# Kernel optimization log

Hardware: AMD Instinct MI355X
Metric: run time of the kernel (lower is better)

The kernel has to match this reference:

```python
import jax, jax.numpy as jnp
import numpy as np

# dims (see shape_source)
B, NC, DIM_IN = 4, 4095, 64      # batch, cells, invariant state dim (n-6)
D, H, L, K = 128, 4, 2, 6        # d_model, heads, layers, num_neighbors
DH = D // H                      # dim_head = 32
HR, NRBF = 16, 16                # radial hidden dim (d_model//8), rbf basis
RBF_MAX, RBF_W = 4.0, 0.25


def _ln(x, s, b):
    m = x.mean(-1, keepdims=True)
    v = x.var(-1, keepdims=True)
    return (x - m) / jnp.sqrt(v + 1e-5) * s + b


def setup_inputs() -> dict:
    key = jax.random.key(0)
    ks = jax.random.split(key, 32)
    def nrm(k, shape, scale):
        return jax.random.normal(k, shape, jnp.float32) * scale
    p = {}
    p['X'] = nrm(ks[0], (B, NC, 6 + DIM_IN), 1.0)
    p['W_embed'] = nrm(ks[1], (DIM_IN, D), DIM_IN ** -0.5)
    p['b_embed'] = jnp.zeros((D,), jnp.float32)
    p['Wq'] = nrm(ks[2], (L, D, D), D ** -0.5)
    p['Wk'] = nrm(ks[3], (L, D, D), D ** -0.5)
    p['Wv'] = nrm(ks[4], (L, D, D), D ** -0.5)
    p['Wvv'] = nrm(ks[5], (L, D, D), D ** -0.5)
    p['rw1'] = nrm(ks[6], (L, NRBF, HR), NRBF ** -0.5)
    p['rb1'] = jnp.zeros((L, HR), jnp.float32)
    p['rw2'] = nrm(ks[7], (L, HR, 2 * D), HR ** -0.5)
    p['rb2'] = jnp.zeros((L, 2 * D), jnp.float32)
    p['Wo'] = nrm(ks[8], (L, D, D), D ** -0.5)
    p['Wov'] = nrm(ks[9], (L, D, D), D ** -0.5)
    p['ff_w1'] = nrm(ks[10], (L, D, 2 * D), D ** -0.5)
    p['ff_b1'] = jnp.zeros((L, 2 * D), jnp.float32)
    p['ff_w2'] = nrm(ks[11], (L, 2 * D, D), (2 * D) ** -0.5)
    p['ff_b2'] = jnp.zeros((L, D), jnp.float32)
    p['gate_w'] = nrm(ks[12], (L, D, D), D ** -0.5)
    p['gate_b'] = jnp.zeros((L, D), jnp.float32)
    p['ln1_s'] = jnp.ones((L, D), jnp.float32)
    p['ln1_b'] = jnp.zeros((L, D), jnp.float32)
    p['ln2_s'] = jnp.ones((L, D), jnp.float32)
    p['ln2_b'] = jnp.zeros((L, D), jnp.float32)
    p['W_state'] = nrm(ks[13], (D, DIM_IN), D ** -0.5)
    p['b_state'] = jnp.zeros((DIM_IN,), jnp.float32)
    p['W_force'] = nrm(ks[14], (D, 1), D ** -0.5)
    p['b_force'] = jnp.zeros((1,), jnp.float32)
    return p


def _forward(X, W_embed, b_embed, Wq, Wk, Wv, Wvv, rw1, rb1, rw2, rb2, Wo, Wov,
             ff_w1, ff_b1, ff_w2, ff_b2, gate_w, gate_b,
             ln1_s, ln1_b, ln2_s, ln2_b, W_state, b_state, W_force, b_force):
    N = NC + 1  # one extra zero node prepended, as in the torch wrapper
    pos = jnp.concatenate([jnp.zeros((B, 1, 3), X.dtype), X[:, :, 0:3]], axis=1)       # [B,N,3]
    feats = jnp.concatenate([jnp.zeros((B, 1, DIM_IN), X.dtype), X[:, :, 6:]], axis=1)  # [B,N,dim_in]

    # k-nearest-neighbor graph (indices are non-differentiable constants)
    d2 = jnp.sum((pos[:, :, None, :] - pos[:, None, :, :]) ** 2, axis=-1)  # [B,N,N]
    d2 = d2 + jnp.eye(N, dtype=X.dtype) * 1e9                               # exclude self
    _, idx = jax.lax.top_k(-d2, K)                                           # [B,N,K]

    gat = lambda a: jax.vmap(lambda ai, ii: ai[ii])(a, idx)  # [B,N,...] -> [B,N,K,...]

    rel = gat(pos) - pos[:, :, None, :]                      # [B,N,K,3]
    dist = jnp.sqrt(jnp.sum(rel ** 2, axis=-1) + 1e-8)       # [B,N,K]
    u = rel / dist[..., None]                                # unit vectors (degree-1 SH)
    centers = jnp.linspace(0.0, RBF_MAX, NRBF).astype(X.dtype)
    rbf = jnp.exp(-((dist[..., None] - centers) / RBF_W) ** 2)  # [B,N,K,NRBF]

    x0 = feats @ W_embed + b_embed                           # type-0 (invariant) feats
    x1 = jnp.zeros((B, N, D, 3), X.dtype)                    # type-1 (vector) feats

    for l in range(L):
        h = _ln(x0, ln1_s[l], ln1_b[l])
        q = (h @ Wq[l]).reshape(B, N, H, DH)
        kj = gat(h @ Wk[l]).reshape(B, N, K, H, DH)
        vj = gat(h @ Wv[l])                                   # [B,N,K,D]
        # radial MLP on distances -> invariant edge weights
        rad = jax.nn.silu(rbf @ rw1[l] + rb1[l]) @ rw2[l] + rb2[l]  # [B,N,K,2D]
        rg, rv = rad[..., :D], rad[..., D:]
        bias = rg.reshape(B, N, K, H, DH).mean(-1)            # [B,N,K,H]
        logits = jnp.einsum('bnhd,bnkhd->bnhk', q, kj) / np.float32(np.sqrt(DH))
        logits = logits + bias.transpose(0, 1, 3, 2)
        attn = jax.nn.softmax(logits, axis=-1)                # over K neighbors
        # degree-0 messages
        m0 = (vj * jax.nn.silu(rv)).reshape(B, N, K, H, DH)
        out0 = jnp.einsum('bnhk,bnkhd->bnhd', attn, m0).reshape(B, N, D)
        x0 = x0 + out0 @ Wo[l]
        # degree-1 messages: channel-mixed neighbor vectors + radial-weighted unit dirs
        x1j = gat(x1)                                          # [B,N,K,D,3]
        m1 = jnp.einsum('bnkdc,de->bnkec', x1j, Wvv[l]) + rv[..., None] * u[:, :, :, None, :]
        m1 = m1.reshape(B, N, K, H, DH, 3)
        out1 = jnp.einsum('bnhk,bnkhdc->bnhdc', attn, m1).reshape(B, N, D, 3)
        x1 = x1 + jnp.einsum('bndc,de->bnec', out1, Wov[l])
        # feed-forward on invariants + invariant gating of vectors (equivariant)
        h2 = _ln(x0, ln2_s[l], ln2_b[l])
        x0 = x0 + jax.nn.silu(h2 @ ff_w1[l] + ff_b1[l]) @ ff_w2[l] + ff_b2[l]
        x1 = x1 * jax.nn.sigmoid(h2 @ gate_w[l] + gate_b[l])[..., None]

    y0 = x0[:, 1:]                                            # drop extra node
    y1 = jnp.swapaxes(x1[:, 1:], -1, -2)                      # [B,NC,3,D]
    state_update = y0 @ W_state + b_state                     # [B,NC,dim_in]
    forces = (y1 @ W_force + b_force)[..., 0]                 # [B,NC,3]
    forces = forces - forces.mean(axis=1, keepdims=True)      # remove net force
    return state_update, forces


def reference(X, W_embed, b_embed, Wq, Wk, Wv, Wvv, rw1, rb1, rw2, rb2, Wo, Wov,
              ff_w1, ff_b1, ff_w2, ff_b2, gate_w, gate_b,
              ln1_s, ln1_b, ln2_s, ln2_b, W_state, b_state, W_force, b_force):
    return _forward(X, W_embed, b_embed, Wq, Wk, Wv, Wvv, rw1, rb1, rw2, rb2, Wo, Wov,
                    ff_w1, ff_b1, ff_w2, ff_b2, gate_w, gate_b,
                    ln1_s, ln1_b, ln2_s, ln2_b, W_state, b_state, W_force, b_force)
```

## Files before the change

kernel.cpp:

```cpp
#include <hip/hip_runtime.h>
#include <cstdint>
#include <cstddef>

namespace {

constexpr int B_ = 4, NC_ = 4095, N_ = 4096, DIN_ = 64, D_ = 128, K_ = 6;
constexpr int XROW_ = 6 + DIN_;
constexpr int ROWS_ = B_ * N_;
constexpr int KNQ = 4;
constexpr int KCAP = 32;

typedef unsigned short u16;
typedef unsigned int u32;
typedef unsigned long long u64;
typedef __attribute__((ext_vector_type(8))) short short8;
typedef __attribute__((ext_vector_type(8))) unsigned short ushort8;
typedef __attribute__((ext_vector_type(4))) float f32x4;

__device__ __forceinline__ float sigm(float x) { return 1.f / (1.f + expf(-x)); }
__device__ __forceinline__ float silu(float x) { return x / (1.f + expf(-x)); }
__device__ __forceinline__ u16 f2bf(float x) {
    u32 u = __float_as_uint(x);
    u += 0x7FFFu + ((u >> 16) & 1u);
    return (u16)(u >> 16);
}
__device__ __forceinline__ float bf2f(u16 x) {
    return __uint_as_float(((u32)x) << 16);
}

__global__ void k_prep(const float* __restrict__ X, float4* __restrict__ pos4,
                       u16* __restrict__ featsb)
{
    int g = blockIdx.x * 256 + threadIdx.x;
    if (g >= ROWS_ * 64) return;
    int c = g & 63, row = g >> 6;
    int b = row >> 12, n = row & (N_ - 1);
    const float* xr = X + (size_t)(b * NC_ + n - 1) * XROW_;
    featsb[g] = (n > 0) ? f2bf(xr[6 + c]) : (u16)0;
    if (c == 0) {
        float4 p = {0.f, 0.f, 0.f, 0.f};
        if (n > 0) { p.x = xr[0]; p.y = xr[1]; p.z = xr[2]; }
        pos4[row] = p;
    }
}

__device__ __forceinline__ u64 shflxor64(u64 v, int mask)
{
    int lo = __shfl_xor((int)(u32)(v & 0xffffffffull), mask, 64);
    int hi = __shfl_xor((int)(u32)(v >> 32), mask, 64);
    return ((u64)(u32)hi << 32) | (u32)lo;
}

__device__ __forceinline__ float kth6min(float v)
{
    const float BIG = 3.4e38f;
    float kth = BIG;
    #pragma unroll
    for (int r = 0; r < 6; ++r) {
        float m = v;
        #pragma unroll
        for (int off = 1; off < 64; off <<= 1) m = fminf(m, __shfl_xor(m, off, 64));
        kth = m;
        if (v == m) v = BIG;
    }
    return kth;
}

__device__ __forceinline__ void geom_write(const float4* __restrict__ pb, int q, int j,
                                           size_t e, float* __restrict__ uv,
                                           float* __restrict__ rbfv)
{
    float4 pj = pb[j], pn = pb[q];
    float rx = pj.x - pn.x, ry = pj.y - pn.y, rz = pj.z - pn.z;
    float dist = sqrtf(rx * rx + ry * ry + rz * rz + 1e-8f);
    float inv = 1.f / dist;
    uv[e * 3 + 0] = rx * inv; uv[e * 3 + 1] = ry * inv; uv[e * 3 + 2] = rz * inv;
    #pragma unroll
    for (int r = 0; r < 16; ++r) {
        float t = (dist - (4.0f / 15.0f) * r) * 4.0f;
        rbfv[e * 16 + r] = expf(-t * t);
    }
}

__global__ __launch_bounds__(256) void k_knn(const float4* __restrict__ pos4,
                                             int* __restrict__ idxv,
                                             float* __restrict__ uv,
                                             float* __restrict__ rbfv)
{
    __shared__ u64 sHits[4][KNQ][KCAP];
    __shared__ int sCnt[4][KNQ];
    const int w = threadIdx.x >> 6, lane = threadIdx.x & 63;
    const int wave = (blockIdx.x << 2) | w;
    const int b = wave >> 10;
    const int i0 = (wave & 1023) << 2;
    const float4* pb = pos4 + (size_t)b * N_;
    const float BIG = 3.4e38f;

    if (lane < KNQ) sCnt[w][lane] = 0;
    __syncthreads();

    float4 qv[KNQ];
    #pragma unroll
    for (int qq = 0; qq < KNQ; ++qq) qv[qq] = pb[i0 + qq];

    float dmin[KNQ];
    #pragma unroll
    for (int qq = 0; qq < KNQ; ++qq) dmin[qq] = BIG;
    #pragma unroll 4
    for (int it = 0; it < 64; ++it) {
        int j = lane + (it << 6);
        float4 p = pb[j];
        #pragma unroll
        for (int qq = 0; qq < KNQ; ++qq) {
            float dx = p.x - qv[qq].x, dy = p.y - qv[qq].y, dz = p.z - qv[qq].z;
            float dd = dx * dx + dy * dy + dz * dz;
            if (j != i0 + qq) dmin[qq] = fminf(dmin[qq], dd);
        }
    }
    float T[KNQ];
    #pragma unroll
    for (int qq = 0; qq < KNQ; ++qq) T[qq] = kth6min(dmin[qq]) * 1.000002f;

    #pragma unroll 4
    for (int it = 0; it < 64; ++it) {
        int j = lane + (it << 6);
        float4 p = pb[j];
        #pragma unroll
        for (int qq = 0; qq < KNQ; ++qq) {
            float dx = p.x - qv[qq].x, dy = p.y - qv[qq].y, dz = p.z - qv[qq].z;
            float dd = dx * dx + dy * dy + dz * dz;
            if (dd <= T[qq] && j != i0 + qq) {
                int slot = atomicAdd(&sCnt[w][qq], 1);
                if (slot < KCAP)
                    sHits[w][qq][slot] = ((u64)__float_as_uint(dd) << 32) | (u32)j;
            }
        }
    }
    __syncthreads();

    const int g = lane >> 4, li = lane & 15;
    const int cnt = sCnt[w][g];
    const int q = i0 + g;
    u64 ent[KCAP / 16];
    #pragma unroll
    for (int e = 0; e < KCAP / 16; ++e) {
        int slot = li + e * 16;
        ent[e] = (slot < (cnt < KCAP ? cnt : KCAP)) ? sHits[w][g][slot] : ~0ull;
    }
    int myj = -1;
    #pragma unroll
    for (int k = 0; k < 6; ++k) {
        u64 m = ent[0];
        #pragma unroll
        for (int e = 1; e < KCAP / 16; ++e) m = (ent[e] < m) ? ent[e] : m;
        #pragma unroll
        for (int off = 1; off < 16; off <<= 1) {
            u64 o = shflxor64(m, off);
            if (o < m) m = o;
        }
        if (li == k) myj = (int)(u32)(m & 0xffffffffull);
        #pragma unroll
        for (int e = 0; e < KCAP / 16; ++e) if (ent[e] == m) ent[e] = ~0ull;
    }
    if (cnt <= KCAP && li < 6) {
        size_t e = (size_t)(b * N_ + q) * 6 + li;
        idxv[e] = myj;
        geom_write(pb, q, myj, e, uv, rbfv);
    }

    u64 ovf = __ballot(li == 0 && cnt > KCAP);
    while (ovf) {
        int gl = __ffsll(ovf) - 1; ovf &= ovf - 1;
        int qq = gl >> 4;
        int qx = i0 + qq;
        float4 qp = pb[qx];
        float Tq = T[0];
        #pragma unroll
        for (int z = 1; z < KNQ; ++z) if (z == qq) Tq = T[z];
        float e0 = BIG, e1 = BIG, e2 = BIG, e3 = BIG, e4 = BIG, e5 = BIG;
        int j0 = 0, j1 = 0, j2 = 0, j3 = 0, j4 = 0, j5 = 0;
        for (int it = 0; it < 64; ++it) {
            int j = lane + (it << 6);
            float4 p = pb[j];
            float dx = p.x - qp.x, dy = p.y - qp.y, dz = p.z - qp.z;
            float dd = dx * dx + dy * dy + dz * dz;
            if (dd <= Tq && j != qx && dd < e5) {
                e5 = dd; j5 = j;
                float td; int tj;
                if (e5 < e4) { td = e4; e4 = e5; e5 = td; tj = j4; j4 = j5; j5 = tj; }
                if (e4 < e3) { td = e3; e3 = e4; e4 = td; tj = j3; j3 = j4; j4 = tj; }
                if (e3 < e2) { td = e2; e2 = e3; e3 = td; tj = j2; j2 = j3; j3 = tj; }
                if (e2 < e1) { td = e1; e1 = e2; e2 = td; tj = j1; j1 = j2; j2 = tj; }
                if (e1 < e0) { td = e0; e0 = e1; e1 = td; tj = j0; j0 = j1; j1 = tj; }
            }
        }
        u64 a0 = ((u64)__float_as_uint(e0) << 32) | (u32)j0;
        u64 a1 = ((u64)__float_as_uint(e1) << 32) | (u32)j1;
        u64 a2 = ((u64)__float_as_uint(e2) << 32) | (u32)j2;
        u64 a3 = ((u64)__float_as_uint(e3) << 32) | (u32)j3;
        u64 a4 = ((u64)__float_as_uint(e4) << 32) | (u32)j4;
        u64 a5 = ((u64)__float_as_uint(e5) << 32) | (u32)j5;
        int fj = -1;
        #pragma unroll
        for (int k = 0; k < 6; ++k) {
            u64 m = a0;
            #pragma unroll
            for (int off = 1; off < 64; off <<= 1) {
                u64 o = shflxor64(m, off);
                if (o < m) m = o;
            }
            if (a0 == m) { a0 = a1; a1 = a2; a2 = a3; a3 = a4; a4 = a5; a5 = ~0ull; }
            if (lane == k) fj = (int)(u32)(m & 0xffffffffull);
        }
        if (lane < 6) {
            size_t e = (size_t)(b * N_ + qx) * 6 + lane;
            idxv[e] = fj;
            geom_write(pb, qx, fj, e, uv, rbfv);
        }
    }
}

__global__ void k_prepw(const float* __restrict__ Wq, const float* __restrict__ Wk,
                        const float* __restrict__ Wv, const float* __restrict__ gw,
                        const float* __restrict__ fw1, const float* __restrict__ gb_,
                        const float* __restrict__ fb1, const float* __restrict__ Wvv,
                        const float* __restrict__ Wov, const float* __restrict__ Wo_,
                        const float* __restrict__ fw2, const float* __restrict__ rw2,
                        const float* __restrict__ rb2, const float* __restrict__ W_embed,
                        const float* __restrict__ rw1,
                        u16* __restrict__ WqkvT, u16* __restrict__ Wc2T,
                        u16* __restrict__ WvvT, u16* __restrict__ WovT,
                        u16* __restrict__ WoT, u16* __restrict__ fw2T,
                        u16* __restrict__ WembT,
                        float* __restrict__ bias2, float* __restrict__ rwg,
                        float* __restrict__ rw1T, float* __restrict__ rw2vT)
{
    const int l = blockIdx.y;
    int g = blockIdx.x * 256 + threadIdx.x;
    const float* Wq_l = Wq + l * 16384;  const float* Wk_l = Wk + l * 16384;
    const float* Wv_l = Wv + l * 16384;  const float* gw_l = gw + l * 16384;
    const float* fw1_l = fw1 + l * 32768; const float* gb_l = gb_ + l * 128;
    const float* fb1_l = fb1 + l * 256;  const float* Wvv_l = Wvv + l * 16384;
    const float* Wov_l = Wov + l * 16384; const float* Wo_ll = Wo_ + l * 16384;
    const float* fw2_l = fw2 + l * 32768; const float* rw2_l = rw2 + l * 4096;
    const float* rb2_l = rb2 + l * 256;  const float* rw1_l = rw1 + l * 256;

    if (g < 49152) {
        int n = g >> 7, k = g & 127;
        const float* src = (n < 128) ? Wq_l : ((n < 256) ? Wk_l : Wv_l);
        WqkvT[l * 49152 + g] = f2bf(src[k * 128 + (n & 127)]); return;
    }
    g -= 49152;
    if (g < 49152) {
        int n = g >> 7, k = g & 127;
        Wc2T[l * 49152 + g] = f2bf((n < 128) ? gw_l[k * 128 + n] : fw1_l[k * 256 + (n - 128)]); return;
    }
    g -= 49152;
    if (g < 16384) { int n = g >> 7, k = g & 127; WvvT[l * 16384 + g] = f2bf(Wvv_l[k * 128 + n]); return; }
    g -= 16384;
    if (g < 16384) { int n = g >> 7, k = g & 127; WovT[l * 16384 + g] = f2bf(Wov_l[k * 128 + n]); return; }
    g -= 16384;
    if (g < 16384) { int n = g >> 7, k = g & 127; WoT[l * 16384 + g] = f2bf(Wo_ll[k * 128 + n]); return; }
    g -= 16384;
    if (g < 32768) { int n = g >> 8, k = g & 255; fw2T[l * 32768 + g] = f2bf(fw2_l[k * 128 + n]); return; }
    g -= 32768;
    if (g < 384) { bias2[l * 384 + g] = (g < 128) ? gb_l[g] : fb1_l[g - 128]; return; }
    g -= 384;
    if (g < 64) {
        int hh = g >> 2, h = g & 3;
        float a = 0.f;
        #pragma unroll
        for (int dh = 0; dh < 32; ++dh) a += rw2_l[hh * 256 + h * 32 + dh];
        rwg[l * 128 + g] = a * (1.f / 32.f); return;
    }
    g -= 64;
    if (g < 4) {
        float a = 0.f;
        #pragma unroll
        for (int dh = 0; dh < 32; ++dh) a += rb2_l[g * 32 + dh];
        rwg[l * 128 + 64 + g] = a * (1.f / 32.f); return;
    }
    g -= 4;
    if (g < 256) {
        int hh = g >> 4, rr = g & 15;
        rw1T[l * 256 + hh * 16 + rr] = rw1_l[rr * 16 + hh]; return;
    }
    g -= 256;
    if (g < 2048) {
        int t = g >> 4, hh = g & 15;
        rw2vT[l * 2048 + t * 16 + hh] = rw2_l[hh * 256 + 128 + t]; return;
    }
    g -= 2048;
    if (g < 8192 && l == 0) {
        int n = g >> 6, k = g & 63;
        WembT[g] = f2bf(W_embed[k * 128 + n]);
    }
}

template<int KD, int EPI, bool LN, bool X1ACC>
__global__ __launch_bounds__(256) void k_mgemm(
    const u16* __restrict__ A, const u16* __restrict__ WT,
    const float* __restrict__ bias, const float* __restrict__ aux,
    float* __restrict__ C, u16* __restrict__ Cb, int ldc,
    const float* __restrict__ lns, const float* __restrict__ lnb,
    u16* __restrict__ lnout)
{
    __shared__ u16 sA[64 * 40];
    __shared__ u16 sB[128 * 40];
    const int tid = threadIdx.x;
    const int lane = tid & 63, wn = tid >> 6;
    const int m0 = blockIdx.x * 64, n0 = blockIdx.y * 128;
    f32x4 acc[4][2] = {};

    for (int k0 = 0; k0 < KD; k0 += 32) {
        __syncthreads();
        {
            int row = tid >> 2, gk = tid & 3;
            *(uint4*)&sA[row * 40 + gk * 8] =
                *(const uint4*)&A[(size_t)(m0 + row) * KD + k0 + gk * 8];
        }
        #pragma unroll
        for (int cc = 0; cc < 2; ++cc) {
            int c = tid * 2 + cc;
            int row = c >> 2, gk = c & 3;
            *(uint4*)&sB[row * 40 + gk * 8] =
                *(const uint4*)&WT[(size_t)(n0 + row) * KD + k0 + gk * 8];
        }
        __syncthreads();
        const int gk = lane >> 4, lr = lane & 15;
        short8 af[4], bfr[2];
        #pragma unroll
        for (int i = 0; i < 4; ++i)
            af[i] = *(const short8*)&sA[(i * 16 + lr) * 40 + gk * 8];
        #pragma unroll
        for (int i = 0; i < 2; ++i)
            bfr[i] = *(const short8*)&sB[(wn * 32 + i * 16 + lr) * 40 + gk * 8];
        #pragma unroll
        for (int mi = 0; mi < 4; ++mi)
            #pragma unroll
            for (int ni = 0; ni < 2; ++ni)
                acc[mi][ni] = __builtin_amdgcn_mfma_f32_16x16x32_bf16(af[mi], bfr[ni], acc[mi][ni], 0, 0, 0);
    }

    const int lg = lane >> 4;
    const int lc = lane & 15;
    if (LN) {
        __shared__ float sLN[64][4][2];
        float s1[4][4], s2[4][4];
        #pragma unroll
        for (int mi = 0; mi < 4; ++mi) {
            int rbase = m0 + mi * 16 + lg * 4;
            #pragma unroll
            for (int ee = 0; ee < 4; ++ee) { s1[mi][ee] = 0.f; s2[mi][ee] = 0.f; }
            #pragma unroll
            for (int ni = 0; ni < 2; ++ni) {
                int col = wn * 32 + ni * 16 + lc;
                float bc = bias ? bias[col] : 0.f;
                #pragma unroll
                for (int ee = 0; ee < 4; ++ee) {
                    float v = acc[mi][ni][ee] + bc;
                    if (EPI == 1) v += C[(size_t)(rbase + ee) * 128 + col];
                    acc[mi][ni][ee] = v;
                    s1[mi][ee] += v;
                    s2[mi][ee] += v * v;
                }
            }
        }
        #pragma unroll
        for (int mi = 0; mi < 4; ++mi)
            #pragma unroll
            for (int ee = 0; ee < 4; ++ee)
                #pragma unroll
                for (int off = 1; off < 16; off <<= 1) {
                    s1[mi][ee] += __shfl_xor(s1[mi][ee], off, 64);
                    s2[mi][ee] += __shfl_xor(s2[mi][ee], off, 64);
                }
        if (lc == 0) {
            #pragma unroll
            for (int mi = 0; mi < 4; ++mi)
                #pragma unroll
                for (int ee = 0; ee < 4; ++ee) {
                    int r = mi * 16 + lg * 4 + ee;
                    sLN[r][wn][0] = s1[mi][ee];
                    sLN[r][wn][1] = s2[mi][ee];
                }
        }
        __syncthreads();
        #pragma unroll
        for (int mi = 0; mi < 4; ++mi) {
            int rbase = m0 + mi * 16 + lg * 4;
            #pragma unroll
            for (int ee = 0; ee < 4; ++ee) {
                int r = mi * 16 + lg * 4 + ee;
                float sum = sLN[r][0][0] + sLN[r][1][0] + sLN[r][2][0] + sLN[r][3][0];
                float sq  = sLN[r][0][1] + sLN[r][1][1] + sLN[r][2][1] + sLN[r][3][1];
                float mean = sum * (1.f / 128.f);
                float var = sq * (1.f / 128.f) - mean * mean;
                float inv = 1.f / sqrtf(var + 1e-5f);
                #pragma unroll
                for (int ni = 0; ni < 2; ++ni) {
                    int col = wn * 32 + ni * 16 + lc;
                    float v = acc[mi][ni][ee];
                    size_t o = (size_t)(rbase + ee) * 128 + col;
                    C[o] = v;
                    lnout[o] = f2bf((v - mean) * inv * lns[col] + lnb[col]);
                }
            }
        }
        return;
    }

    #pragma unroll
    for (int mi = 0; mi < 4; ++mi) {
        int rbase = m0 + mi * 16 + lg * 4;
        #pragma unroll
        for (int ni = 0; ni < 2; ++ni) {
            int col = n0 + wn * 32 + ni * 16 + lc;
            if (EPI == 0) {
                float bc = bias ? bias[col] : 0.f;
                #pragma unroll
                for (int ee = 0; ee < 4; ++ee)
                    C[(size_t)(rbase + ee) * ldc + col] = acc[mi][ni][ee] + bc;
            } else if (EPI == 1) {
                float bc = bias ? bias[col] : 0.f;
                #pragma unroll
                for (int ee = 0; ee < 4; ++ee) {
                    size_t o = (size_t)(rbase + ee) * ldc + col;
                    C[o] += acc[mi][ni][ee] + bc;
                }
            } else if (EPI == 2) {
                float bc = bias[col];
                if (n0 == 0) {
                    #pragma unroll
                    for (int ee = 0; ee < 4; ++ee)
                        C[(size_t)(rbase + ee) * 128 + col] = sigm(acc[mi][ni][ee] + bc);
                } else {
                    int c2 = col - 128;
                    #pragma unroll
                    for (int ee = 0; ee < 4; ++ee)
                        Cb[(size_t)(rbase + ee) * 256 + c2] = f2bf(silu(acc[mi][ni][ee] + bc));
                }
            } else if (EPI == 4) {
                float bc = bias ? bias[col] : 0.f;
                #pragma unroll
                for (int ee = 0; ee < 4; ++ee)
                    Cb[(size_t)(rbase + ee) * ldc + col] = f2bf(acc[mi][ni][ee] + bc);
            } else {
                #pragma unroll
                for (int ee = 0; ee < 4; ++ee) {
                    int m = rbase + ee;
                    size_t o = (size_t)m * 128 + col;
                    float v = acc[mi][ni][ee];
                    if (X1ACC) v += C[o];
                    v *= aux[(size_t)(m / 3) * 128 + col];
                    C[o] = v;
                    Cb[o] = f2bf(v);
                }
            }
        }
    }
}

template<int KD>
__global__ __launch_bounds__(256) void k_tgemm(
    const float* __restrict__ A, const float* __restrict__ W, const float* __restrict__ bias,
    float* __restrict__ C, int ldw, int ldc)
{
    __shared__ __align__(16) float As[32 * 132];
    __shared__ __align__(16) float Ws[32 * 68];
    const int tid = threadIdx.x;
    const int tx = tid & 15, ty = tid >> 4;
    const int m0 = blockIdx.x * 128, n0 = blockIdx.y * 64;
    float acc[8][4] = {};
    for (int k0 = 0; k0 < KD; k0 += 32) {
        __syncthreads();
        #pragma unroll
        for (int r = 0; r < 4; ++r) {
            int id = tid + r * 256;
            int row = id >> 3, kq = id & 7;
            float4 a4 = *(const float4*)&A[(size_t)(m0 + row) * KD + k0 + kq * 4];
            As[(kq * 4 + 0) * 132 + row] = a4.x;
            As[(kq * 4 + 1) * 132 + row] = a4.y;
            As[(kq * 4 + 2) * 132 + row] = a4.z;
            As[(kq * 4 + 3) * 132 + row] = a4.w;
        }
        #pragma unroll
        for (int r = 0; r < 2; ++r) {
            int id = tid + r * 256;
            int kr = id >> 4, cq = id & 15;
            *(float4*)&Ws[kr * 68 + cq * 4] =
                *(const float4*)&W[(size_t)(k0 + kr) * ldw + n0 + cq * 4];
        }
        __syncthreads();
        #pragma unroll 8
        for (int k = 0; k < 32; ++k) {
            float4 aA = *(const float4*)&As[k * 132 + ty * 8];
            float4 aB = *(const float4*)&As[k * 132 + ty * 8 + 4];
            float4 w4 = *(const float4*)&Ws[k * 68 + tx * 4];
            float av[8] = {aA.x, aA.y, aA.z, aA.w, aB.x, aB.y, aB.z, aB.w};
            float wv[4] = {w4.x, w4.y, w4.z, w4.w};
            #pragma unroll
            for (int r = 0; r < 8; ++r)
                #pragma unroll
                for (int j = 0; j < 4; ++j)
                    acc[r][j] += av[r] * wv[j];
        }
    }
    float bv[4];
    #pragma unroll
    for (int j = 0; j < 4; ++j) bv[j] = bias[n0 + tx * 4 + j];
    #pragma unroll
    for (int r = 0; r < 8; ++r) {
        int m = m0 + ty * 8 + r;
        int n = m & (N_ - 1), bb2 = m >> 12;
        if (n == 0) continue;
        float* dst = C + ((size_t)(bb2 * NC_ + n - 1)) * ldc + n0 + tx * 4;
        float4 res = {acc[r][0] + bv[0], acc[r][1] + bv[1], acc[r][2] + bv[2], acc[r][3] + bv[3]};
        *(float4*)dst = res;
    }
}

template<bool HASY1>
__global__ __launch_bounds__(256) void k_attn(
    const u16* __restrict__ qkvb, const int* __restrict__ idxv,
    const float* __restrict__ rbfv, const float* __restrict__ uv,
    const u16* __restrict__ y1b,
    const float* __restrict__ rw1T, const float* __restrict__ rb1,
    const float* __restrict__ rw2vT, const float* __restrict__ rwg,
    const float* __restrict__ rb2,
    u16* __restrict__ o0b, u16* __restrict__ o1b)
{
    const int tid = threadIdx.x;
    const int r = tid >> 7, t = tid & 127;
    const int row = blockIdx.x * 2 + r;
    const int b = row >> 12;

    __shared__ float sQ[2][128];
    __shared__ float sHid[2][6][16];
    __shared__ float sU[2][6][3];
    __shared__ float sLog[2][4][6];
    __shared__ float sAttn[2][4][6];
    __shared__ int sJ[2][6];

    sQ[r][t] = bf2f(qkvb[(size_t)row * 384 + t]);
    if (t < 6) sJ[r][t] = idxv[row * 6 + t];
    if (t >= 8 && t < 26) { int i = t - 8; sU[r][i / 3][i % 3] = uv[(size_t)row * 18 + i]; }
    if (t >= 32) {
        int k = (t - 32) >> 4, hh = (t - 32) & 15;
        float a = rb1[hh];
        const float* rb = rbfv + (size_t)(row * 6 + k) * 16;
        const float* wr = rw1T + hh * 16;
        #pragma unroll
        for (int rr = 0; rr < 16; ++rr) a += rb[rr] * wr[rr];
        sHid[r][k][hh] = silu(a);
    }
    __syncthreads();

    if (t < 96) {
        int g = t >> 2, o = t & 3;
        int h = g / 6, k = g - h * 6;
        const u16* kp = qkvb + (size_t)(b * N_ + sJ[r][k]) * 384 + 128 + h * 32 + o * 8;
        ushort8 kk = *(const ushort8*)kp;
        float p = 0.f;
        #pragma unroll
        for (int i = 0; i < 8; ++i)
            p += sQ[r][h * 32 + o * 8 + i] * bf2f(kk[i]);
        p += __shfl_down(p, 2, 4);
        p += __shfl_down(p, 1, 4);
        if (o == 0) {
            float bias = rwg[64 + h];
            #pragma unroll
            for (int hh = 0; hh < 16; ++hh) bias += sHid[r][k][hh] * rwg[hh * 4 + h];
            sLog[r][h][k] = p * 0.17677669529663687f + bias;
        }
    }
    float rwc[16];
    {
        const float4* wp = (const float4*)(rw2vT + t * 16);
        float4 w0 = wp[0], w1 = wp[1], w2 = wp[2], w3 = wp[3];
        rwc[0]=w0.x; rwc[1]=w0.y; rwc[2]=w0.z; rwc[3]=w0.w;
        rwc[4]=w1.x; rwc[5]=w1.y; rwc[6]=w1.z; rwc[7]=w1.w;
        rwc[8]=w2.x; rwc[9]=w2.y; rwc[10]=w2.z; rwc[11]=w2.w;
        rwc[12]=w3.x; rwc[13]=w3.y; rwc[14]=w3.z; rwc[15]=w3.w;
    }
    float rvk[6], vj[6], y1j[6][3];
    float rb2t = rb2[128 + t];
    #pragma unroll
    for (int k = 0; k < 6; ++k) {
        float a = rb2t;
        #pragma unroll
        for (int hh = 0; hh < 16; ++hh) a += sHid[r][k][hh] * rwc[hh];
        rvk[k] = a;
        size_t nb = (size_t)(b * N_ + sJ[r][k]);
        vj[k] = bf2f(qkvb[nb * 384 + 256 + t]);
        if (HASY1) {
            #pragma unroll
            for (int c = 0; c < 3; ++c) y1j[k][c] = bf2f(y1b[(nb * 3 + c) * 128 + t]);
        }
    }
    __syncthreads();

    if (t < 4) {
        int h = t;
        float mx = sLog[r][h][0];
        #pragma unroll
        for (int k = 1; k < 6; ++k) mx = fmaxf(mx, sLog[r][h][k]);
        float ex[6], smv = 0.f;
        #pragma unroll
        for (int k = 0; k < 6; ++k) { ex[k] = expf(sLog[r][h][k] - mx); smv += ex[k]; }
        float inv = 1.f / smv;
        #pragma unroll
        for (int k = 0; k < 6; ++k) sAttn[r][h][k] = ex[k] * inv;
    }
    __syncthreads();

    int h = t >> 5;
    float a[6];
    #pragma unroll
    for (int k = 0; k < 6; ++k) a[k] = sAttn[r][h][k];
    float o0v = 0.f;
    #pragma unroll
    for (int k = 0; k < 6; ++k) o0v += a[k] * vj[k] * silu(rvk[k]);
    o0b[(size_t)row * 128 + t] = f2bf(o0v);
    #pragma unroll
    for (int c = 0; c < 3; ++c) {
        float s = 0.f;
        #pragma unroll
        for (int k = 0; k < 6; ++k) {
            float base = HASY1 ? y1j[k][c] : 0.f;
            s += a[k] * (base + rvk[k] * sU[r][k][c]);
        }
        o1b[(size_t)(row * 3 + c) * 128 + t] = f2bf(s);
    }
}

__global__ void k_force1(const float* __restrict__ x1, const float* __restrict__ W,
                         const float* __restrict__ bias, float* __restrict__ frc)
{
    int g = blockIdx.x * 256 + threadIdx.x;
    if (g >= B_ * NC_ * 3) return;
    int c = g % 3, rr = g / 3;
    int b = rr / NC_, n = rr - b * NC_;
    const float* xr = x1 + (size_t)(b * N_ + n + 1) * 384 + c * 128;
    float a = bias[0];
    for (int d = 0; d < 128; ++d) a += xr[d] * W[d];
    frc[g] = a;
}

__global__ __launch_bounds__(256) void k_fsum(const float* __restrict__ frc, float* __restrict__ fsum)
{
    int b = blockIdx.x / 3, c = blockIdx.x % 3;
    __shared__ float red[256];
    float a = 0.f;
    for (int n = threadIdx.x; n < NC_; n += 256) a += frc[(b * NC_ + n) * 3 + c];
    red[threadIdx.x] = a; __syncthreads();
    for (int st = 128; st > 0; st >>= 1) { if (threadIdx.x < st) red[threadIdx.x] += red[threadIdx.x + st]; __syncthreads(); }
    if (threadIdx.x == 0) fsum[blockIdx.x] = red[0] / (float)NC_;
}

__global__ void k_force2(const float* __restrict__ frc, const float* __restrict__ fsum,
                         float* __restrict__ out)
{
    int g = blockIdx.x * 256 + threadIdx.x;
    if (g >= B_ * NC_ * 3) return;
    int c = g % 3;
    int b = g / (NC_ * 3);
    out[g] = frc[g] - fsum[b * 3 + c];
}

}

extern "C" void kernel_launch(void* const* d_in, const int* in_sizes, int n_in,
                              void* d_out, int out_size, void* d_ws, size_t ws_size,
                              hipStream_t stream)
{
    const float* X       = (const float*)d_in[0];
    const float* W_embed = (const float*)d_in[1];
    const float* b_embed = (const float*)d_in[2];
    const float* Wq      = (const float*)d_in[3];
    const float* Wk      = (const float*)d_in[4];
    const float* Wv      = (const float*)d_in[5];
    const float* Wvv     = (const float*)d_in[6];
    const float* rw1     = (const float*)d_in[7];
    const float* rb1     = (const float*)d_in[8];
    const float* rw2     = (const float*)d_in[9];
    const float* rb2     = (const float*)d_in[10];
    const float* Wo      = (const float*)d_in[11];
    const float* Wov     = (const float*)d_in[12];
    const float* ff_w1   = (const float*)d_in[13];
    const float* ff_b1   = (const float*)d_in[14];
    const float* ff_w2   = (const float*)d_in[15];
    const float* ff_b2   = (const float*)d_in[16];
    const float* gate_w  = (const float*)d_in[17];
    const float* gate_b  = (const float*)d_in[18];
    const float* ln1_s   = (const float*)d_in[19];
    const float* ln1_b   = (const float*)d_in[20];
    const float* ln2_s   = (const float*)d_in[21];
    const float* ln2_b   = (const float*)d_in[22];
    const float* W_state = (const float*)d_in[23];
    const float* b_state = (const float*)d_in[24];
    const float* W_force = (const float*)d_in[25];
    const float* b_force = (const float*)d_in[26];
    (void)in_sizes; (void)n_in; (void)out_size; (void)ws_size;

    float* out = (float*)d_out;
    float* w = (float*)d_ws;

    float4* pos4  = (float4*)w;
    int*    idxv  = (int*)(w + 65536);
    float*  uv    = w + 163840;
    float*  rbfv  = w + 458752;
    u16*    featsb= (u16*)(w + 2031616);
    float*  x0    = w + 2555904;
    u16*    hbb   = (u16*)(w + 4653056);
    u16*    qkvbb = (u16*)(w + 5701632);
    float*  gb    = w + 11993088;
    u16*    o0b   = (u16*)(w + 14090240);
    u16*    o1b   = (u16*)(w + 15138816);
    float*  x1    = w + 18284544;
    u16*    x1b   = (u16*)(w + 24576000);
    u16*    t1b   = (u16*)(w + 27721728);
    u16*    y1b   = t1b;
    u16*    WqkvT = (u16*)(w + 34013184);
    u16*    Wc2T  = (u16*)(w + 34062336);
    u16*    WvvT  = (u16*)(w + 34111488);
    u16*    WovT  = (u16*)(w + 34127872);
    u16*    WoT   = (u16*)(w + 34144256);
    u16*    fw2T  = (u16*)(w + 34160640);
    u16*    WembT = (u16*)(w + 34193408);
    float*  bias2 = w + 34197504;
    float*  rwg   = w + 34198272;
    float*  rw1T  = w + 34198528;
    float*  rw2vT = w + 34199040;
    float*  frc   = (float*)featsb;
    float*  fsum  = ((float*)featsb) + 49152;

    k_prepw<<<dim3(747, 2), 256, 0, stream>>>(Wq, Wk, Wv, gate_w, ff_w1, gate_b, ff_b1,
                                              Wvv, Wov, Wo, ff_w2, rw2, rb2, W_embed, rw1,
                                              WqkvT, Wc2T, WvvT, WovT, WoT, fw2T, WembT,
                                              bias2, rwg, rw1T, rw2vT);
    k_prep<<<(ROWS_ * 64 + 255) / 256, 256, 0, stream>>>(X, pos4, featsb);
    k_knn<<<ROWS_ / 16, 256, 0, stream>>>(pos4, idxv, uv, rbfv);
    k_mgemm<64, 0, true, true><<<dim3(256, 1), 256, 0, stream>>>(
        featsb, WembT, b_embed, nullptr, x0, nullptr, 128, ln1_s, ln1_b, hbb);

    for (int l = 0; l < 2; ++l) {
        const float* rb1_l = rb1 + l * 16;
        const float* rb2_l = rb2 + l * 256;
        const float* fb2_l = ff_b2 + l * 128;

        k_mgemm<128, 4, false, true><<<dim3(256, 3), 256, 0, stream>>>(
            hbb, WqkvT + l * 49152, nullptr, nullptr, nullptr, qkvbb, 384, nullptr, nullptr, nullptr);
        if (l > 0)
            k_mgemm<128, 4, false, true><<<dim3(768, 1), 256, 0, stream>>>(
                x1b, WvvT + l * 16384, nullptr, nullptr, nullptr, y1b, 128, nullptr, nullptr, nullptr);
        if (l == 0)
            k_attn<false><<<ROWS_ / 2, 256, 0, stream>>>(qkvbb, idxv, rbfv, uv, nullptr,
                rw1T + l * 256, rb1_l, rw2vT + l * 2048, rwg + l * 128, rb2_l, o0b, o1b);
        else
            k_attn<true><<<ROWS_ / 2, 256, 0, stream>>>(qkvbb, idxv, rbfv, uv, y1b,
                rw1T + l * 256, rb1_l, rw2vT + l * 2048, rwg + l * 128, rb2_l, o0b, o1b);
        k_mgemm<128, 1, true, true><<<dim3(256, 1), 256, 0, stream>>>(
            o0b, WoT + l * 16384, nullptr, nullptr, x0, nullptr, 128,
            ln2_s + l * 128, ln2_b + l * 128, hbb);
        k_mgemm<128, 2, false, true><<<dim3(256, 3), 256, 0, stream>>>(
            hbb, Wc2T + l * 49152, bias2 + l * 384, nullptr, gb, t1b, 128, nullptr, nullptr, nullptr);
        if (l == 0)
            k_mgemm<128, 3, false, false><<<dim3(768, 1), 256, 0, stream>>>(
                o1b, WovT + l * 16384, nullptr, gb, x1, x1b, 128, nullptr, nullptr, nullptr);
        else
            k_mgemm<128, 3, false, true><<<dim3(768, 1), 256, 0, stream>>>(
                o1b, WovT + l * 16384, nullptr, gb, x1, x1b, 128, nullptr, nullptr, nullptr);
        if (l == 0)
            k_mgemm<256, 1, true, true><<<dim3(256, 1), 256, 0, stream>>>(
                t1b, fw2T + l * 32768, fb2_l, nullptr, x0, nullptr, 128,
                ln1_s + 128, ln1_b + 128, hbb);
        else
            k_mgemm<256, 1, false, true><<<dim3(256, 1), 256, 0, stream>>>(
                t1b, fw2T + l * 32768, fb2_l, nullptr, x0, nullptr, 128, nullptr, nullptr, nullptr);
    }

    k_tgemm<128><<<dim3(128, 1), 256, 0, stream>>>(x0, W_state, b_state, out, 64, 64);
    k_force1<<<(B_ * NC_ * 3 + 255) / 256, 256, 0, stream>>>(x1, W_force, b_force, frc);
    k_fsum<<<12, 256, 0, stream>>>(frc, fsum);
    k_force2<<<(B_ * NC_ * 3 + 255) / 256, 256, 0, stream>>>(frc, fsum, out + (size_t)B_ * NC_ * DIN_);
}
```

Before: 351.6 us.

## Restructure neighbor attention to one wavefront per row with shuffle reductions

```diff
diff --git a/kernel.cpp b/kernel.cpp
--- a/kernel.cpp
+++ b/kernel.cpp
@@ -530,107 +530,125 @@
     const float* __restrict__ rb2,
     u16* __restrict__ o0b, u16* __restrict__ o1b)
 {
-    const int tid = threadIdx.x;
-    const int r = tid >> 7, t = tid & 127;
-    const int row = blockIdx.x * 2 + r;
+    const int wid = threadIdx.x >> 6, lane = threadIdx.x & 63;
+    const int row = blockIdx.x * 4 + wid;
     const int b = row >> 12;
-
-    __shared__ float sQ[2][128];
-    __shared__ float sHid[2][6][16];
-    __shared__ float sU[2][6][3];
-    __shared__ float sLog[2][4][6];
-    __shared__ float sAttn[2][4][6];
-    __shared__ int sJ[2][6];
-
-    sQ[r][t] = bf2f(qkvb[(size_t)row * 384 + t]);
-    if (t < 6) sJ[r][t] = idxv[row * 6 + t];
-    if (t >= 8 && t < 26) { int i = t - 8; sU[r][i / 3][i % 3] = uv[(size_t)row * 18 + i]; }
-    if (t >= 32) {
-        int k = (t - 32) >> 4, hh = (t - 32) & 15;
-        float a = rb1[hh];
-        const float* rb = rbfv + (size_t)(row * 6 + k) * 16;
-        const float* wr = rw1T + hh * 16;
-        #pragma unroll
-        for (int rr = 0; rr < 16; ++rr) a += rb[rr] * wr[rr];
-        sHid[r][k][hh] = silu(a);
-    }
-    __syncthreads();
-
-    if (t < 96) {
-        int g = t >> 2, o = t & 3;
-        int h = g / 6, k = g - h * 6;
-        const u16* kp = qkvb + (size_t)(b * N_ + sJ[r][k]) * 384 + 128 + h * 32 + o * 8;
-        ushort8 kk = *(const ushort8*)kp;
-        float p = 0.f;
-        #pragma unroll
-        for (int i = 0; i < 8; ++i)
-            p += sQ[r][h * 32 + o * 8 + i] * bf2f(kk[i]);
-        p += __shfl_down(p, 2, 4);
-        p += __shfl_down(p, 1, 4);
-        if (o == 0) {
-            float bias = rwg[64 + h];
-            #pragma unroll
-            for (int hh = 0; hh < 16; ++hh) bias += sHid[r][k][hh] * rwg[hh * 4 + h];
-            sLog[r][h][k] = p * 0.17677669529663687f + bias;
-        }
-    }
-    float rwc[16];
+    const int ch0 = lane * 2;
+    const int h = lane >> 4;
+
+    __shared__ float sHid[4][6][16];
+    __shared__ float sU[4][6][3];
+
+    int jl = 0;
+    if (lane < 6) jl = idxv[row * 6 + lane];
+    int jj[6];
+    #pragma unroll
+    for (int k = 0; k < 6; ++k) jj[k] = __shfl(jl, k, 64);
+
+    if (lane < 18) sU[wid][lane / 3][lane % 3] = uv[(size_t)row * 18 + lane];
+
     {
-        const float4* wp = (const float4*)(rw2vT + t * 16);
-        float4 w0 = wp[0], w1 = wp[1], w2 = wp[2], w3 = wp[3];
-        rwc[0]=w0.x; rwc[1]=w0.y; rwc[2]=w0.z; rwc[3]=w0.w;
-        rwc[4]=w1.x; rwc[5]=w1.y; rwc[6]=w1.z; rwc[7]=w1.w;
-        rwc[8]=w2.x; rwc[9]=w2.y; rwc[10]=w2.z; rwc[11]=w2.w;
-        rwc[12]=w3.x; rwc[13]=w3.y; rwc[14]=w3.z; rwc[15]=w3.w;
-    }
-    float rvk[6], vj[6], y1j[6][3];
-    float rb2t = rb2[128 + t];
+        int idx = lane;
+        #pragma unroll
+        for (int rep = 0; rep < 2; ++rep) {
+            if (idx < 96) {
+                int k = idx >> 4, hh = idx & 15;
+                float a = rb1[hh];
+                const float* rb = rbfv + (size_t)(row * 6 + k) * 16;
+                const float* wr = rw1T + hh * 16;
+                #pragma unroll
+                for (int rr = 0; rr < 16; ++rr) a += rb[rr] * wr[rr];
+                sHid[wid][k][hh] = silu(a);
+            }
+            idx += 64;
+        }
+    }
+    __builtin_amdgcn_wave_barrier();
+    __threadfence_block();
+    __builtin_amdgcn_wave_barrier();
+
+    u32 qp = *(const u32*)&qkvb[(size_t)row * 384 + ch0];
+    float q0 = bf2f((u16)qp), q1 = bf2f((u16)(qp >> 16));
+
+    float part[6];
     #pragma unroll
     for (int k = 0; k < 6; ++k) {
-        float a = rb2t;
-        #pragma unroll
-        for (int hh = 0; hh < 16; ++hh) a += sHid[r][k][hh] * rwc[hh];
-        rvk[k] = a;
-        size_t nb = (size_t)(b * N_ + sJ[r][k]);
-        vj[k] = bf2f(qkvb[nb * 384 + 256 + t]);
-        if (HASY1) {
-            #pragma unroll
-            for (int c = 0; c < 3; ++c) y1j[k][c] = bf2f(y1b[(nb * 3 + c) * 128 + t]);
-        }
-    }
-    __syncthreads();
-
-    if (t < 4) {
-        int h = t;
-        float mx = sLog[r][h][0];
-        #pragma unroll
-        for (int k = 1; k < 6; ++k) mx = fmaxf(mx, sLog[r][h][k]);
-        float ex[6], smv = 0.f;
-        #pragma unroll
-        for (int k = 0; k < 6; ++k) { ex[k] = expf(sLog[r][h][k] - mx); smv += ex[k]; }
-        float inv = 1.f / smv;
-        #pragma unroll
-        for (int k = 0; k < 6; ++k) sAttn[r][h][k] = ex[k] * inv;
-    }
-    __syncthreads();
-
-    int h = t >> 5;
-    float a[6];
-    #pragma unroll
-    for (int k = 0; k < 6; ++k) a[k] = sAttn[r][h][k];
-    float o0v = 0.f;
-    #pragma unroll
-    for (int k = 0; k < 6; ++k) o0v += a[k] * vj[k] * silu(rvk[k]);
-    o0b[(size_t)row * 128 + t] = f2bf(o0v);
+        u32 kp = *(const u32*)&qkvb[(size_t)(b * N_ + jj[k]) * 384 + 128 + ch0];
+        part[k] = q0 * bf2f((u16)kp) + q1 * bf2f((u16)(kp >> 16));
+    }
+    #pragma unroll
+    for (int off = 1; off < 16; off <<= 1)
+        #pragma unroll
+        for (int k = 0; k < 6; ++k)
+            part[k] += __shfl_xor(part[k], off, 64);
+
+    float lg[6];
+    #pragma unroll
+    for (int k = 0; k < 6; ++k) {
+        float bias = rwg[64 + h];
+        #pragma unroll
+        for (int hh = 0; hh < 16; ++hh) bias += sHid[wid][k][hh] * rwg[hh * 4 + h];
+        lg[k] = part[k] * 0.17677669529663687f + bias;
+    }
+
+    float mx = lg[0];
+    #pragma unroll
+    for (int k = 1; k < 6; ++k) mx = fmaxf(mx, lg[k]);
+    float a[6], smv = 0.f;
+    #pragma unroll
+    for (int k = 0; k < 6; ++k) { a[k] = expf(lg[k] - mx); smv += a[k]; }
+    float inv = 1.f / smv;
+    #pragma unroll
+    for (int k = 0; k < 6; ++k) a[k] *= inv;
+
+    float rwc0[16], rwc1[16];
+    {
+        const float4* wp = (const float4*)(rw2vT + ch0 * 16);
+        #pragma unroll
+        for (int i = 0; i < 4; ++i) {
+            float4 v0 = wp[i], v1 = wp[i + 4];
+            rwc0[i * 4 + 0] = v0.x; rwc0[i * 4 + 1] = v0.y; rwc0[i * 4 + 2] = v0.z; rwc0[i * 4 + 3] = v0.w;
+            rwc1[i * 4 + 0] = v1.x; rwc1[i * 4 + 1] = v1.y; rwc1[i * 4 + 2] = v1.z; rwc1[i * 4 + 3] = v1.w;
+        }
+    }
+    float rb20 = rb2[128 + ch0], rb21 = rb2[128 + ch0 + 1];
+    float rvk0[6], rvk1[6];
+    #pragma unroll
+    for (int k = 0; k < 6; ++k) {
+        float a0 = rb20, a1 = rb21;
+        #pragma unroll
+        for (int hh = 0; hh < 16; ++hh) {
+            float hv = sHid[wid][k][hh];
+            a0 += hv * rwc0[hh];
+            a1 += hv * rwc1[hh];
+        }
+        rvk0[k] = a0; rvk1[k] = a1;
+    }
+
+    float o00 = 0.f, o01 = 0.f;
+    #pragma unroll
+    for (int k = 0; k < 6; ++k) {
+        u32 vp = *(const u32*)&qkvb[(size_t)(b * N_ + jj[k]) * 384 + 256 + ch0];
+        o00 += a[k] * bf2f((u16)vp) * silu(rvk0[k]);
+        o01 += a[k] * bf2f((u16)(vp >> 16)) * silu(rvk1[k]);
+    }
+    *(u32*)&o0b[(size_t)row * 128 + ch0] = (u32)f2bf(o00) | ((u32)f2bf(o01) << 16);
+
     #pragma unroll
     for (int c = 0; c < 3; ++c) {
-        float s = 0.f;
+        float s0 = 0.f, s1 = 0.f;
         #pragma unroll
         for (int k = 0; k < 6; ++k) {
-            float base = HASY1 ? y1j[k][c] : 0.f;
-            s += a[k] * (base + rvk[k] * sU[r][k][c]);
-        }
-        o1b[(size_t)(row * 3 + c) * 128 + t] = f2bf(s);
+            float b0 = 0.f, b1 = 0.f;
+            if (HASY1) {
+                u32 yp = *(const u32*)&y1b[((size_t)(b * N_ + jj[k]) * 3 + c) * 128 + ch0];
+                b0 = bf2f((u16)yp); b1 = bf2f((u16)(yp >> 16));
+            }
+            float uk = sU[wid][k][c];
+            s0 += a[k] * (b0 + rvk0[k] * uk);
+            s1 += a[k] * (b1 + rvk1[k] * uk);
+        }
+        *(u32*)&o1b[((size_t)row * 3 + c) * 128 + ch0] = (u32)f2bf(s0) | ((u32)f2bf(s1) << 16);
     }
 }
 
@@ -755,10 +773,10 @@
             k_mgemm<128, 4, false, true><<<dim3(768, 1), 256, 0, stream>>>(
                 x1b, WvvT + l * 16384, nullptr, nullptr, nullptr, y1b, 128, nullptr, nullptr, nullptr);
         if (l == 0)
-            k_attn<false><<<ROWS_ / 2, 256, 0, stream>>>(qkvbb, idxv, rbfv, uv, nullptr,
+            k_attn<false><<<ROWS_ / 4, 256, 0, stream>>>(qkvbb, idxv, rbfv, uv, nullptr,
                 rw1T + l * 256, rb1_l, rw2vT + l * 2048, rwg + l * 128, rb2_l, o0b, o1b);
         else
-            k_attn<true><<<ROWS_ / 2, 256, 0, stream>>>(qkvbb, idxv, rbfv, uv, y1b,
+            k_attn<true><<<ROWS_ / 4, 256, 0, stream>>>(qkvbb, idxv, rbfv, uv, y1b,
                 rw1T + l * 256, rb1_l, rw2vT + l * 2048, rwg + l * 128, rb2_l, o0b, o1b);
         k_mgemm<128, 1, true, true><<<dim3(256, 1), 256, 0, stream>>>(
             o0b, WoT + l * 16384, nullptr, nullptr, x0, nullptr, 128,
```

Result: faster. 330.8 us (-5.9%).
